# Performance work log

Hardware: AMD Instinct MI355X
Metric: run time of the kernel (lower is better)

The kernel has to match this reference:

```python
import jax, jax.numpy as jnp
import numpy as np
from jax import lax

LIN_DIMS = [(3200, 2048), (2048, 1024), (1024, 512), (512, 256), (256, 128),
            (128, 64), (64, 32), (32, 16), (16, 8), (8, 4), (4, 2), (2, 1)]
BN_EPS = 1e-5


def _conv(x, w, b):
    y = lax.conv_general_dilated(x, w, window_strides=(3, 3),
                                 padding=((1, 1), (1, 1)),
                                 dimension_numbers=('NCHW', 'OIHW', 'NCHW'))
    return y + b.reshape(1, -1, 1, 1)


def _bn(x, g, b):
    # training-mode BatchNorm2d: biased batch statistics over (N, H, W)
    m = jnp.mean(x, axis=(0, 2, 3), keepdims=True)
    v = jnp.var(x, axis=(0, 2, 3), keepdims=True)
    return (x - m) * lax.rsqrt(v + BN_EPS) * g.reshape(1, -1, 1, 1) + b.reshape(1, -1, 1, 1)


def setup_inputs() -> dict:
    key = jax.random.key(0)
    ks = iter(jax.random.split(key, 64))
    d = {}
    d['x'] = jax.random.normal(next(ks), (64, 512, 40, 40), jnp.float32)
    d['conv1_w'] = jax.random.normal(next(ks), (256, 512, 3, 3), jnp.float32) / np.sqrt(512 * 9)
    d['conv1_b'] = jnp.zeros((256,), jnp.float32)
    d['bn1_g'] = jnp.ones((256,), jnp.float32)
    d['bn1_b'] = jnp.zeros((256,), jnp.float32)
    d['conv2_w'] = jax.random.normal(next(ks), (128, 256, 3, 3), jnp.float32) / np.sqrt(256 * 9)
    d['conv2_b'] = jnp.zeros((128,), jnp.float32)
    d['bn2_g'] = jnp.ones((128,), jnp.float32)
    d['bn2_b'] = jnp.zeros((128,), jnp.float32)
    for i, (fin, fout) in enumerate(LIN_DIMS):
        d[f'w{i+3}'] = jax.random.normal(next(ks), (fout, fin), jnp.float32) / np.sqrt(fin)
        d[f'b{i+3}'] = jax.random.normal(next(ks), (fout,), jnp.float32) * 0.01
    return d


def reference(x, conv1_w, conv1_b, bn1_g, bn1_b, conv2_w, conv2_b, bn2_g, bn2_b,
              w3, b3, w4, b4, w5, b5, w6, b6, w7, b7, w8, b8, w9, b9,
              w10, b10, w11, b11, w12, b12, w13, b13, w14, b14):
    h = _bn(_conv(x, conv1_w, conv1_b), bn1_g, bn1_b)          # [B,256,14,14]
    h = _bn(_conv(h, conv2_w, conv2_b), bn2_g, bn2_b)          # [B,128,5,5]
    h = h.reshape(h.shape[0], 3200)
    for w, b in [(w3, b3), (w4, b4), (w5, b5), (w6, b6), (w7, b7), (w8, b8),
                 (w9, b9), (w10, b10), (w11, b11), (w12, b12), (w13, b13), (w14, b14)]:
        h = h @ w.T + b
    return jax.nn.sigmoid(h)                                   # [B,1]
```

## Files before the change

### kernel.cpp

```cpp
#include <hip/hip_runtime.h>
#include <cstdint>
#include <cstddef>

typedef short bf16x8 __attribute__((ext_vector_type(8)));
typedef float f32x4 __attribute__((ext_vector_type(4)));

__device__ __forceinline__ unsigned short f2bf(float f) {
  union { float f; unsigned u; } v; v.f = f;
  unsigned r = v.u + 0x7fffu + ((v.u >> 16) & 1u);
  return (unsigned short)(r >> 16);
}

#define GLOAD_LDS16(gp, lp)                                            \
  __builtin_amdgcn_global_load_lds(                                    \
      (const __attribute__((address_space(1))) void*)(const void*)(gp),\
      (__attribute__((address_space(3))) void*)(void*)(lp), 16, 0, 0)

__global__ __launch_bounds__(256) void cast1(const float* __restrict__ w1,
                                             unsigned short* __restrict__ W1r) {
  int idx = blockIdx.x * 256 + threadIdx.x;
  int co = idx >> 9, ci = idx & 511;
  const float* src = w1 + (size_t)idx * 9;
#pragma unroll
  for (int r = 0; r < 9; ++r)
    W1r[(size_t)co * 4608 + r * 512 + ci] = f2bf(src[r]);
}

__global__ __launch_bounds__(256) void transpose_x(const float* __restrict__ x,
                                                   unsigned short* __restrict__ xT) {
  __shared__ float lds[64 * 41];
  int t = threadIdx.x;
  int cc = blockIdx.x, ihp = blockIdx.y, img = blockIdx.z;
  int ih = ihp - 1;
  bool rowvalid = (unsigned)ih < 40u;
  if (rowvalid) {
    for (int idx = t; idx < 640; idx += 256) {
      int row = idx / 10, q = idx - row * 10;
      float4 v = *(const float4*)(x + (((size_t)img * 512 + cc * 64 + row) * 40 + ih) * 40 + q * 4);
      float* d = lds + row * 41 + q * 4;
      d[0] = v.x; d[1] = v.y; d[2] = v.z; d[3] = v.w;
    }
  }
  __syncthreads();
  for (int idx = t; idx < 672; idx += 256) {
    int iwp = idx >> 4, u = idx & 15;
    int iw = iwp - 1;
    bool ok = rowvalid && (unsigned)iw < 40u;
    ushort4 o;
    unsigned short vv[4];
#pragma unroll
    for (int j = 0; j < 4; ++j)
      vv[j] = ok ? f2bf(lds[(u * 4 + j) * 41 + iw]) : (unsigned short)0;
    o.x = vv[0]; o.y = vv[1]; o.z = vv[2]; o.w = vv[3];
    *(ushort4*)(xT + (((size_t)img * 42 + ihp) * 42 + iwp) * 512 + cc * 64 + u * 4) = o;
  }
}

__global__ __launch_bounds__(256) void gemm1_fused(const unsigned short* __restrict__ xT,
                                                   const unsigned short* __restrict__ W1r,
                                                   unsigned short* __restrict__ A2,
                                                   float* __restrict__ SUM1,
                                                   float* __restrict__ SQ1) {
  __shared__ __align__(16) unsigned short As[4 * 64 * 32];
  __shared__ __align__(16) unsigned short Bs[4 * 64 * 32];
  int t = threadIdx.x;
  int m0 = blockIdx.x * 64;
  int n0 = blockIdx.y * 64;
  int arow = m0 + (t >> 2);
  int img_s = arow / 196, sp_s = arow - img_s * 196;
  int oh_s = sp_s / 14, ow_s = sp_s - oh_s * 14;
  const unsigned short* Abase =
      xT + (((size_t)img_s * 42 + 3 * oh_s) * 42 + 3 * ow_s) * 512 + (t & 3) * 8;
  const unsigned short* Bbase = W1r + (size_t)(n0 + (t >> 2)) * 4608 + (t & 3) * 8;
  int q = (t & 63) >> 4, mr = t & 15;
  int wm = ((t >> 6) & 1) * 32;
  int wn = (t >> 7) * 32;
  f32x4 acc[2][2] = {};

  for (int kc = 0; kc < 36; ++kc) {
    int r = kc >> 2;
    int kh = (r >= 6) ? 2 : (r >= 3 ? 1 : 0);
    int kw = r - 3 * kh;
    int aoff = (kh * 42 + kw) * 512 + (kc & 3) * 128;
    int boff = kc * 128;
    __syncthreads();
#pragma unroll
    for (int i = 0; i < 4; ++i) {
      GLOAD_LDS16(Abase + aoff + i * 32, As + (i * 256 + t) * 8);
      GLOAD_LDS16(Bbase + boff + i * 32, Bs + (i * 256 + t) * 8);
    }
    __syncthreads();
#pragma unroll
    for (int ks = 0; ks < 4; ++ks) {
      bf16x8 af[2], bfr[2];
#pragma unroll
      for (int s = 0; s < 2; ++s)
        af[s] = *((const bf16x8*)(As + ks * 2048 + (wm + s * 16 + mr) * 32 + q * 8));
#pragma unroll
      for (int nt = 0; nt < 2; ++nt)
        bfr[nt] = *((const bf16x8*)(Bs + ks * 2048 + (wn + nt * 16 + mr) * 32 + q * 8));
#pragma unroll
      for (int nt = 0; nt < 2; ++nt)
#pragma unroll
        for (int s = 0; s < 2; ++s)
          acc[s][nt] = __builtin_amdgcn_mfma_f32_16x16x32_bf16(af[s], bfr[nt], acc[s][nt], 0, 0, 0);
    }
  }

#pragma unroll
  for (int nt = 0; nt < 2; ++nt) {
    float cs = 0.f, cq = 0.f;
#pragma unroll
    for (int s = 0; s < 2; ++s)
#pragma unroll
      for (int rr = 0; rr < 4; ++rr) {
        float v = acc[s][nt][rr];
        cs += v; cq += v * v;
      }
    cs += __shfl_xor(cs, 16, 64); cq += __shfl_xor(cq, 16, 64);
    cs += __shfl_xor(cs, 32, 64); cq += __shfl_xor(cq, 32, 64);
    if (q == 0) {
      int col = n0 + wn + nt * 16 + mr;
      atomicAdd(&SUM1[col], cs);
      atomicAdd(&SQ1[col], cq);
    }
  }

#pragma unroll
  for (int s = 0; s < 2; ++s)
#pragma unroll
    for (int rr = 0; rr < 4; ++rr) {
      int m = m0 + wm + s * 16 + q * 4 + rr;
      int img = m / 196, sp = m - img * 196;
      int oh1 = sp / 14, ow1 = sp - oh1 * 14;
      int oh2 = (oh1 + 1) / 3, kh2 = (oh1 + 1) - 3 * oh2;
      int ow2 = (ow1 + 1) / 3, kw2 = (ow1 + 1) - 3 * ow2;
      size_t dst = (size_t)(img * 25 + oh2 * 5 + ow2) * 2304 + (kh2 * 3 + kw2) * 256;
#pragma unroll
      for (int nt = 0; nt < 2; ++nt)
        A2[dst + n0 + wn + nt * 16 + mr] = f2bf(acc[s][nt][rr]);
    }
}

__global__ __launch_bounds__(256) void prep2(const float* __restrict__ w2,
                                             const float* __restrict__ g1,
                                             const float* __restrict__ b1,
                                             const float* __restrict__ SUM1,
                                             const float* __restrict__ SQ1,
                                             unsigned short* __restrict__ W2s,
                                             float* __restrict__ T4) {
  int bid = blockIdx.x, t = threadIdx.x;
  if (bid < 128) {
    int idx = bid * 256 + t;
    int co = idx >> 8, ci = idx & 255;
    float mean = SUM1[ci] * (1.f / 12544.f);
    float var = SQ1[ci] * (1.f / 12544.f) - mean * mean;
    float sc = g1[ci] * rsqrtf(var + 1e-5f);
    const float* src = w2 + (size_t)idx * 9;
#pragma unroll
    for (int r = 0; r < 9; ++r)
      W2s[(size_t)co * 2304 + r * 256 + ci] = f2bf(src[r] * sc);
  } else {
    int b2 = bid - 128;
    int cls = b2 >> 7, co = b2 & 127;
    int ci = t;
    float mean = SUM1[ci] * (1.f / 12544.f);
    float var = SQ1[ci] * (1.f / 12544.f) - mean * mean;
    float sc = g1[ci] * rsqrtf(var + 1e-5f);
    float sh = b1[ci] - mean * sc;
    const float* src = w2 + ((size_t)co * 256 + ci) * 9;
    float p = 0.f;
#pragma unroll
    for (int r = 0; r < 9; ++r) {
      int kh = r / 3, kw = r - 3 * kh;
      bool ok = ((cls & 2) || kh > 0) && ((cls & 1) || kw > 0);
      if (ok) p += src[r];
    }
    p *= sh;
    __shared__ float red[256];
    red[t] = p; __syncthreads();
    for (int s = 128; s > 0; s >>= 1) {
      if (t < s) red[t] += red[t + s];
      __syncthreads();
    }
    if (t == 0) T4[cls * 128 + co] = red[0];
  }
}

template <int BKS>
__global__ __launch_bounds__(256) void gemm_bf16(const unsigned short* __restrict__ A,
                                                 const unsigned short* __restrict__ B,
                                                 float* __restrict__ Cp,
                                                 int M, int N, int K, int k_chunk) {
  __shared__ __align__(16) unsigned short As[BKS * 64 * 32];
  __shared__ __align__(16) unsigned short Bs[BKS * 64 * 32];
  int m0 = blockIdx.x * 64;
  int n0 = blockIdx.y * 64;
  Cp += (size_t)blockIdx.z * M * N;
  int k_begin = blockIdx.z * k_chunk;
  int t = threadIdx.x;
  const unsigned short* Abase = A + (size_t)(m0 + (t >> 2)) * K + (t & 3) * 8;
  const unsigned short* Bbase = B + (size_t)(n0 + (t >> 2)) * K + (t & 3) * 8;
  int q = (t & 63) >> 4, mr = t & 15;
  int wm = ((t >> 6) & 1) * 32;
  int wn = (t >> 7) * 32;
  f32x4 acc[2][2] = {};

  for (int k0 = k_begin; k0 < k_begin + k_chunk; k0 += 32 * BKS) {
    __syncthreads();
#pragma unroll
    for (int i = 0; i < BKS; ++i) {
      GLOAD_LDS16(Abase + k0 + i * 32, As + (i * 256 + t) * 8);
      GLOAD_LDS16(Bbase + k0 + i * 32, Bs + (i * 256 + t) * 8);
    }
    __syncthreads();
#pragma unroll
    for (int ks = 0; ks < BKS; ++ks) {
      bf16x8 af[2], bfr[2];
#pragma unroll
      for (int s = 0; s < 2; ++s)
        af[s] = *((const bf16x8*)(As + ks * 2048 + (wm + s * 16 + mr) * 32 + q * 8));
#pragma unroll
      for (int nt = 0; nt < 2; ++nt)
        bfr[nt] = *((const bf16x8*)(Bs + ks * 2048 + (wn + nt * 16 + mr) * 32 + q * 8));
#pragma unroll
      for (int nt = 0; nt < 2; ++nt)
#pragma unroll
        for (int s = 0; s < 2; ++s)
          acc[s][nt] = __builtin_amdgcn_mfma_f32_16x16x32_bf16(af[s], bfr[nt], acc[s][nt], 0, 0, 0);
    }
  }
#pragma unroll
  for (int s = 0; s < 2; ++s)
#pragma unroll
    for (int nt = 0; nt < 2; ++nt)
#pragma unroll
      for (int r = 0; r < 4; ++r)
        Cp[(size_t)(m0 + wm + s * 16 + q * 4 + r) * N + n0 + wn + nt * 16 + mr] = acc[s][nt][r];
}

__global__ void reduce2_k(const float* __restrict__ C2P, const float* __restrict__ T4,
                          float* __restrict__ C2, float* __restrict__ SUM2,
                          float* __restrict__ SQ2) {
  int c = threadIdx.x;
  int r0 = blockIdx.x * 16;
  float s = 0.f, s2 = 0.f;
  for (int r = 0; r < 16; ++r) {
    int m = r0 + r, sp = m % 25;
    int oh = sp / 5, ow = sp - oh * 5;
    int cls = ((oh > 0) ? 2 : 0) | ((ow > 0) ? 1 : 0);
    size_t off = (size_t)m * 128 + c;
    float v = T4[cls * 128 + c];
#pragma unroll
    for (int k = 0; k < 8; ++k) v += C2P[(size_t)k * 204800 + off];
    C2[off] = v;
    s += v; s2 += v * v;
  }
  atomicAdd(&SUM2[c], s);
  atomicAdd(&SQ2[c], s2);
}

__global__ void mlp_head(const float* w14, const float* b14,
                         const float* w13, const float* b13,
                         const float* w12, const float* b12,
                         const float* w11, const float* b11,
                         const float* w10, const float* b10,
                         const float* w9,  const float* b9,
                         const float* w8,  const float* b8,
                         const float* w7,  const float* b7,
                         float* __restrict__ r_out, float* __restrict__ c_out) {
  __shared__ float ra[256], rb[256];
  int t = threadIdx.x;
  float cs = 0.f;
  if (t < 2) ra[t] = w14[t];
  if (t == 0) cs = b14[0];
  __syncthreads();
  const float* Ws[7] = {w13, w12, w11, w10, w9, w8, w7};
  const float* Bs[7] = {b13, b12, b11, b10, b9, b8, b7};
  const int fouts[7] = {2, 4, 8, 16, 32, 64, 128};
  float* cur = ra; float* nxt = rb;
  for (int s = 0; s < 7; ++s) {
    int fo = fouts[s], fi = fo * 2;
    if (t == 0) {
      float d = 0.f;
      for (int i = 0; i < fo; ++i) d += cur[i] * Bs[s][i];
      cs += d;
    }
    if (t < fi) {
      float a = 0.f;
      const float* W = Ws[s];
      for (int i = 0; i < fo; ++i) a += cur[i] * W[i * fi + t];
      nxt[t] = a;
    }
    __syncthreads();
    float* tmp = cur; cur = nxt; nxt = tmp;
  }
  r_out[t] = cur[t];
  if (t == 0) c_out[0] = cs;
}

__global__ void mlp_stage(const float* __restrict__ W, const float* __restrict__ bt,
                          const float* __restrict__ r_in, const float* __restrict__ c_in,
                          float* __restrict__ r_out, float* __restrict__ c_out,
                          int fin, int fout) {
  __shared__ float red[256];
  int t = threadIdx.x;
  int jl = t & 31, ig = t >> 5;
  int j = blockIdx.x * 32 + jl;
  int chunk = fout >> 3;
  int i0 = ig * chunk;
  float acc = 0.f;
  for (int i = i0; i < i0 + chunk; ++i)
    acc += r_in[i] * W[(size_t)i * fin + j];
  red[t] = acc;
  __syncthreads();
  if (ig == 0) {
    float s = 0.f;
#pragma unroll
    for (int u = 0; u < 8; ++u) s += red[u * 32 + jl];
    r_out[j] = s;
  }
  if (blockIdx.x == 0) {
    __syncthreads();
    float p = 0.f;
    for (int i = t; i < fout; i += 256) p += r_in[i] * bt[i];
    red[t] = p;
    __syncthreads();
    for (int s = 128; s > 0; s >>= 1) {
      if (t < s) red[t] += red[t + s];
      __syncthreads();
    }
    if (t == 0) c_out[0] = red[0] + c_in[0];
  }
}

__global__ void final_k(const float* __restrict__ C2, const float* __restrict__ SUM2,
                        const float* __restrict__ SQ2, const float* __restrict__ g2,
                        const float* __restrict__ b2, const float* __restrict__ r,
                        const float* __restrict__ c_in, float* __restrict__ out) {
  int n = blockIdx.x;
  int t = threadIdx.x;
  float acc = 0.f;
  for (int j = t; j < 3200; j += 256) {
    int c = j / 25, sp = j - c * 25;
    float mean = SUM2[c] * (1.f / 1600.f);
    float var = SQ2[c] * (1.f / 1600.f) - mean * mean;
    float sc = g2[c] / sqrtf(var + 1e-5f);
    float sh = b2[c] - mean * sc;
    float v = C2[((size_t)n * 25 + sp) * 128 + c] * sc + sh;
    acc += v * r[j];
  }
  __shared__ float red[256];
  red[t] = acc;
  __syncthreads();
  for (int s = 128; s > 0; s >>= 1) {
    if (t < s) red[t] += red[t + s];
    __syncthreads();
  }
  if (t == 0) {
    float z = red[0] + c_in[0];
    out[n] = 1.f / (1.f + expf(-z));
  }
}

static constexpr size_t OFF_XT   = 0;
static constexpr size_t OFF_A2   = 115605504;
static constexpr size_t OFF_C2P  = 122978304;
static constexpr size_t OFF_C2   = 129531904;
static constexpr size_t OFF_W1R  = 130351104;
static constexpr size_t OFF_W2S  = 132710400;
static constexpr size_t OFF_T4   = 133300224;
static constexpr size_t OFF_STATS= 133302272;
static constexpr size_t OFF_RA   = 133306368;
static constexpr size_t OFF_RB   = 133319424;
static constexpr size_t OFF_CA   = 133332480;
static constexpr size_t OFF_CB   = 133332608;

extern "C" void kernel_launch(void* const* d_in, const int* in_sizes, int n_in,
                              void* d_out, int out_size, void* d_ws, size_t ws_size,
                              hipStream_t stream) {
  const float* x   = (const float*)d_in[0];
  const float* w1  = (const float*)d_in[1];
  const float* g1  = (const float*)d_in[3];
  const float* bb1 = (const float*)d_in[4];
  const float* w2  = (const float*)d_in[5];
  const float* g2  = (const float*)d_in[7];
  const float* bb2 = (const float*)d_in[8];

  char* ws = (char*)d_ws;
  unsigned short* xT  = (unsigned short*)(ws + OFF_XT);
  unsigned short* A2  = (unsigned short*)(ws + OFF_A2);
  float*          C2P = (float*)(ws + OFF_C2P);
  float*          C2  = (float*)(ws + OFF_C2);
  unsigned short* W1r = (unsigned short*)(ws + OFF_W1R);
  unsigned short* W2s = (unsigned short*)(ws + OFF_W2S);
  float*          T4  = (float*)(ws + OFF_T4);
  float* SUM1 = (float*)(ws + OFF_STATS);
  float* SQ1  = (float*)(ws + OFF_STATS + 1024);
  float* SUM2 = (float*)(ws + OFF_STATS + 2048);
  float* SQ2  = (float*)(ws + OFF_STATS + 3072);
  float* RA   = (float*)(ws + OFF_RA);
  float* RB   = (float*)(ws + OFF_RB);
  float* CA   = (float*)(ws + OFF_CA);
  float* CB   = (float*)(ws + OFF_CB);

  hipMemsetAsync(ws + OFF_STATS, 0, 4096, stream);
  hipMemsetAsync(A2, 0, 7372800, stream);

  cast1<<<512, 256, 0, stream>>>(w1, W1r);
  transpose_x<<<dim3(8, 42, 64), 256, 0, stream>>>(x, xT);

  gemm1_fused<<<dim3(196, 4), 256, 0, stream>>>(xT, W1r, A2, SUM1, SQ1);

  prep2<<<640, 256, 0, stream>>>(w2, g1, bb1, SUM1, SQ1, W2s, T4);

  gemm_bf16<3><<<dim3(25, 2, 8), 256, 0, stream>>>(A2, W2s, C2P, 1600, 128, 2304, 288);
  reduce2_k<<<100, 128, 0, stream>>>(C2P, T4, C2, SUM2, SQ2);

  mlp_head<<<1, 256, 0, stream>>>(
      (const float*)d_in[31], (const float*)d_in[32],
      (const float*)d_in[29], (const float*)d_in[30],
      (const float*)d_in[27], (const float*)d_in[28],
      (const float*)d_in[25], (const float*)d_in[26],
      (const float*)d_in[23], (const float*)d_in[24],
      (const float*)d_in[21], (const float*)d_in[22],
      (const float*)d_in[19], (const float*)d_in[20],
      (const float*)d_in[17], (const float*)d_in[18],
      RA, CA);
  mlp_stage<<<16, 256, 0, stream>>>((const float*)d_in[15], (const float*)d_in[16],
                                    RA, CA, RB, CB, 512, 256);
  mlp_stage<<<32, 256, 0, stream>>>((const float*)d_in[13], (const float*)d_in[14],
                                    RB, CB, RA, CA, 1024, 512);
  mlp_stage<<<64, 256, 0, stream>>>((const float*)d_in[11], (const float*)d_in[12],
                                    RA, CA, RB, CB, 2048, 1024);
  mlp_stage<<<100, 256, 0, stream>>>((const float*)d_in[9], (const float*)d_in[10],
                                     RB, CB, RA, CA, 3200, 2048);

  final_k<<<64, 256, 0, stream>>>(C2, SUM2, SQ2, g2, bb2, RA, CA, (float*)d_out);
}
```

Before: 832.5 us.

## Fuse init memsets into cast kernel, swizzle GEMM1 LDS, merge MLP stages

Replaces the two memsets and the weight cast with one init kernel. In the conv1 GEMM, the weight tile is no longer staged in LDS: B fragments are read straight from global/L2, and the A tile in LDS gets an XOR swizzle to avoid bank conflicts. Two more MLP stages move into a single 1024-thread head kernel, which removes two launches. Risks: the direct global B loads may be slower than the LDS path, and the serial chain in the head kernel gets longer.

New measurement: 788.5 us. 5.3% less time.

```diff
diff --git a/kernel.cpp b/kernel.cpp
--- a/kernel.cpp
+++ b/kernel.cpp
@@ -16,14 +16,24 @@
       (const __attribute__((address_space(1))) void*)(const void*)(gp),\
       (__attribute__((address_space(3))) void*)(void*)(lp), 16, 0, 0)
 
-__global__ __launch_bounds__(256) void cast1(const float* __restrict__ w1,
-                                             unsigned short* __restrict__ W1r) {
-  int idx = blockIdx.x * 256 + threadIdx.x;
-  int co = idx >> 9, ci = idx & 511;
-  const float* src = w1 + (size_t)idx * 9;
-#pragma unroll
-  for (int r = 0; r < 9; ++r)
-    W1r[(size_t)co * 4608 + r * 512 + ci] = f2bf(src[r]);
+__global__ __launch_bounds__(256) void init_k(const float* __restrict__ w1,
+                                              unsigned short* __restrict__ W1r,
+                                              unsigned short* __restrict__ A2,
+                                              float* __restrict__ stats) {
+  int bid = blockIdx.x, t = threadIdx.x;
+  if (bid < 512) {
+    int idx = bid * 256 + t;
+    int co = idx >> 9, ci = idx & 511;
+    const float* src = w1 + (size_t)idx * 9;
+#pragma unroll
+    for (int r = 0; r < 9; ++r)
+      W1r[(size_t)co * 4608 + r * 512 + ci] = f2bf(src[r]);
+  } else if (bid < 2312) {
+    int idx = (bid - 512) * 256 + t;
+    ((uint4*)A2)[idx] = make_uint4(0, 0, 0, 0);
+  } else {
+    ((float4*)stats)[t] = make_float4(0.f, 0.f, 0.f, 0.f);
+  }
 }
 
 __global__ __launch_bounds__(256) void transpose_x(const float* __restrict__ x,
@@ -62,19 +72,20 @@
                                                    float* __restrict__ SUM1,
                                                    float* __restrict__ SQ1) {
   __shared__ __align__(16) unsigned short As[4 * 64 * 32];
-  __shared__ __align__(16) unsigned short Bs[4 * 64 * 32];
   int t = threadIdx.x;
   int m0 = blockIdx.x * 64;
   int n0 = blockIdx.y * 64;
-  int arow = m0 + (t >> 2);
+  int R = t >> 2;
+  int p = (t & 3) ^ ((R >> 1) & 3);
+  int arow = m0 + R;
   int img_s = arow / 196, sp_s = arow - img_s * 196;
   int oh_s = sp_s / 14, ow_s = sp_s - oh_s * 14;
   const unsigned short* Abase =
-      xT + (((size_t)img_s * 42 + 3 * oh_s) * 42 + 3 * ow_s) * 512 + (t & 3) * 8;
-  const unsigned short* Bbase = W1r + (size_t)(n0 + (t >> 2)) * 4608 + (t & 3) * 8;
+      xT + (((size_t)img_s * 42 + 3 * oh_s) * 42 + 3 * ow_s) * 512 + p * 8;
   int q = (t & 63) >> 4, mr = t & 15;
   int wm = ((t >> 6) & 1) * 32;
   int wn = (t >> 7) * 32;
+  const unsigned short* Brow = W1r + (size_t)(n0 + wn + mr) * 4608 + q * 8;
   f32x4 acc[2][2] = {};
 
   for (int kc = 0; kc < 36; ++kc) {
@@ -82,23 +93,23 @@
     int kh = (r >= 6) ? 2 : (r >= 3 ? 1 : 0);
     int kw = r - 3 * kh;
     int aoff = (kh * 42 + kw) * 512 + (kc & 3) * 128;
-    int boff = kc * 128;
-    __syncthreads();
-#pragma unroll
-    for (int i = 0; i < 4; ++i) {
+    __syncthreads();
+#pragma unroll
+    for (int i = 0; i < 4; ++i)
       GLOAD_LDS16(Abase + aoff + i * 32, As + (i * 256 + t) * 8);
-      GLOAD_LDS16(Bbase + boff + i * 32, Bs + (i * 256 + t) * 8);
-    }
     __syncthreads();
 #pragma unroll
     for (int ks = 0; ks < 4; ++ks) {
       bf16x8 af[2], bfr[2];
 #pragma unroll
-      for (int s = 0; s < 2; ++s)
-        af[s] = *((const bf16x8*)(As + ks * 2048 + (wm + s * 16 + mr) * 32 + q * 8));
+      for (int s = 0; s < 2; ++s) {
+        int Rr = wm + s * 16 + mr;
+        int ch = Rr * 4 + (q ^ ((Rr >> 1) & 3));
+        af[s] = *((const bf16x8*)(As + ks * 2048 + ch * 8));
+      }
 #pragma unroll
       for (int nt = 0; nt < 2; ++nt)
-        bfr[nt] = *((const bf16x8*)(Bs + ks * 2048 + (wn + nt * 16 + mr) * 32 + q * 8));
+        bfr[nt] = *((const bf16x8*)(Brow + (size_t)nt * 16 * 4608 + kc * 128 + ks * 32));
 #pragma unroll
       for (int nt = 0; nt < 2; ++nt)
 #pragma unroll
@@ -169,16 +180,16 @@
     float sc = g1[ci] * rsqrtf(var + 1e-5f);
     float sh = b1[ci] - mean * sc;
     const float* src = w2 + ((size_t)co * 256 + ci) * 9;
-    float p = 0.f;
+    float pacc = 0.f;
 #pragma unroll
     for (int r = 0; r < 9; ++r) {
       int kh = r / 3, kw = r - 3 * kh;
       bool ok = ((cls & 2) || kh > 0) && ((cls & 1) || kw > 0);
-      if (ok) p += src[r];
-    }
-    p *= sh;
+      if (ok) pacc += src[r];
+    }
+    pacc *= sh;
     __shared__ float red[256];
-    red[t] = p; __syncthreads();
+    red[t] = pacc; __syncthreads();
     for (int s = 128; s > 0; s >>= 1) {
       if (t < s) red[t] += red[t + s];
       __syncthreads();
@@ -260,31 +271,31 @@
   atomicAdd(&SQ2[c], s2);
 }
 
-__global__ void mlp_head(const float* w14, const float* b14,
-                         const float* w13, const float* b13,
-                         const float* w12, const float* b12,
-                         const float* w11, const float* b11,
-                         const float* w10, const float* b10,
-                         const float* w9,  const float* b9,
-                         const float* w8,  const float* b8,
-                         const float* w7,  const float* b7,
-                         float* __restrict__ r_out, float* __restrict__ c_out) {
-  __shared__ float ra[256], rb[256];
-  int t = threadIdx.x;
-  float cs = 0.f;
+__global__ __launch_bounds__(1024) void mlp_head1024(
+    const float* w14, const float* b14, const float* w13, const float* b13,
+    const float* w12, const float* b12, const float* w11, const float* b11,
+    const float* w10, const float* b10, const float* w9,  const float* b9,
+    const float* w8,  const float* b8,  const float* w7,  const float* b7,
+    const float* w6,  const float* b6,  const float* w5,  const float* b5,
+    float* __restrict__ r_out, float* __restrict__ c_out) {
+  __shared__ float ra[1024], rb[1024];
+  __shared__ float csv;
+  int t = threadIdx.x;
   if (t < 2) ra[t] = w14[t];
-  if (t == 0) cs = b14[0];
+  if (t == 0) csv = b14[0];
   __syncthreads();
-  const float* Ws[7] = {w13, w12, w11, w10, w9, w8, w7};
-  const float* Bs[7] = {b13, b12, b11, b10, b9, b8, b7};
-  const int fouts[7] = {2, 4, 8, 16, 32, 64, 128};
+  const float* Ws[9] = {w13, w12, w11, w10, w9, w8, w7, w6, w5};
+  const float* Bs[9] = {b13, b12, b11, b10, b9, b8, b7, b6, b5};
+  const int fouts[9] = {2, 4, 8, 16, 32, 64, 128, 256, 512};
   float* cur = ra; float* nxt = rb;
-  for (int s = 0; s < 7; ++s) {
+  for (int s = 0; s < 9; ++s) {
     int fo = fouts[s], fi = fo * 2;
-    if (t == 0) {
-      float d = 0.f;
-      for (int i = 0; i < fo; ++i) d += cur[i] * Bs[s][i];
-      cs += d;
+    if (t < 64) {
+      float pd = 0.f;
+      for (int i = t; i < fo; i += 64) pd += cur[i] * Bs[s][i];
+#pragma unroll
+      for (int off = 32; off > 0; off >>= 1) pd += __shfl_down(pd, off, 64);
+      if (t == 0) csv += pd;
     }
     if (t < fi) {
       float a = 0.f;
@@ -296,7 +307,7 @@
     float* tmp = cur; cur = nxt; nxt = tmp;
   }
   r_out[t] = cur[t];
-  if (t == 0) c_out[0] = cs;
+  if (t == 0) c_out[0] = csv;
 }
 
 __global__ void mlp_stage(const float* __restrict__ W, const float* __restrict__ bt,
@@ -404,10 +415,8 @@
   float* CA   = (float*)(ws + OFF_CA);
   float* CB   = (float*)(ws + OFF_CB);
 
-  hipMemsetAsync(ws + OFF_STATS, 0, 4096, stream);
-  hipMemsetAsync(A2, 0, 7372800, stream);
-
-  cast1<<<512, 256, 0, stream>>>(w1, W1r);
+  init_k<<<2313, 256, 0, stream>>>(w1, W1r, A2, (float*)(ws + OFF_STATS));
+
   transpose_x<<<dim3(8, 42, 64), 256, 0, stream>>>(x, xT);
 
   gemm1_fused<<<dim3(196, 4), 256, 0, stream>>>(xT, W1r, A2, SUM1, SQ1);
@@ -417,7 +426,7 @@
   gemm_bf16<3><<<dim3(25, 2, 8), 256, 0, stream>>>(A2, W2s, C2P, 1600, 128, 2304, 288);
   reduce2_k<<<100, 128, 0, stream>>>(C2P, T4, C2, SUM2, SQ2);
 
-  mlp_head<<<1, 256, 0, stream>>>(
+  mlp_head1024<<<1, 1024, 0, stream>>>(
       (const float*)d_in[31], (const float*)d_in[32],
       (const float*)d_in[29], (const float*)d_in[30],
       (const float*)d_in[27], (const float*)d_in[28],
@@ -426,15 +435,13 @@
       (const float*)d_in[21], (const float*)d_in[22],
       (const float*)d_in[19], (const float*)d_in[20],
       (const float*)d_in[17], (const float*)d_in[18],
-      RA, CA);
-  mlp_stage<<<16, 256, 0, stream>>>((const float*)d_in[15], (const float*)d_in[16],
-                                    RA, CA, RB, CB, 512, 256);
-  mlp_stage<<<32, 256, 0, stream>>>((const float*)d_in[13], (const float*)d_in[14],
-                                    RB, CB, RA, CA, 1024, 512);
+      (const float*)d_in[15], (const float*)d_in[16],
+      (const float*)d_in[13], (const float*)d_in[14],
+      RB, CB);
   mlp_stage<<<64, 256, 0, stream>>>((const float*)d_in[11], (const float*)d_in[12],
-                                    RA, CA, RB, CB, 2048, 1024);
+                                    RB, CB, RA, CA, 2048, 1024);
   mlp_stage<<<100, 256, 0, stream>>>((const float*)d_in[9], (const float*)d_in[10],
-                                     RB, CB, RA, CA, 3200, 2048);
-
-  final_k<<<64, 256, 0, stream>>>(C2, SUM2, SQ2, g2, bb2, RA, CA, (float*)d_out);
-}
+                                     RA, CA, RB, CB, 3200, 2048);
+
+  final_k<<<64, 256, 0, stream>>>(C2, SUM2, SQ2, g2, bb2, RB, CB, (float*)d_out);
+}
```
